# Kernel optimization log

Measured on AMD Instinct MI355X. Metric: run time of the kernel, lower is better.

The kernel has to match this reference:

```python
import jax, jax.numpy as jnp
import numpy as np

W_PAD = 1  # reflection pad / stencil half-width
CLAMP_MIN = 0.071
EPS = 1e-05


def _laplacian_kernel():
    k = 2 * W_PAD + 1
    ker = -jnp.ones((1, 1, k, k, k), dtype=jnp.float32)
    ker = ker.at[0, 0, W_PAD, W_PAD, W_PAD].set(float(k * k * k - 1))
    return ker  # [O=1, I=1, 3, 3, 3]


def _boundary_weight(pred):
    # pred: [B, L, D, H, W] raw logits
    B, L, D, H, Wd = pred.shape
    ps = jax.nn.softmax(pred, axis=1).astype(jnp.float32)
    # reflect-pad spatial dims by 1, then clamp (matches torch: pad then clamp)
    p = jnp.pad(ps, ((0, 0), (0, 0), (1, 1), (1, 1), (1, 1)), mode='reflect')
    p = jnp.clip(p, CLAMP_MIN)
    # single-channel 3x3x3 stencil applied independently per (batch, label)
    x = p.reshape(B * L, 1, D + 2, H + 2, Wd + 2)
    bt = jax.lax.conv_general_dilated(
        x, _laplacian_kernel(), window_strides=(1, 1, 1), padding='VALID',
        dimension_numbers=('NCDHW', 'OIDHW', 'NCDHW'))
    bt = jnp.abs(bt).reshape(B, L, D, H, Wd)
    bt = jax.lax.stop_gradient(bt)  # torch .detach()
    return 0.5 / (bt + 0.5)


def _dice_bpm(y_pred, y_true, bpm):
    vol_axes = tuple(range(2, y_pred.ndim))  # spatial dims
    top = 2.0 * jnp.sum(y_true * y_pred * bpm, axis=vol_axes)
    bottom = jnp.clip(jnp.sum((y_true + y_pred) * bpm, axis=vol_axes), EPS)
    return -jnp.mean(top / bottom)


def setup_inputs() -> dict:
    key = jax.random.key(0)
    k1, k2 = jax.random.split(key)
    shape = (2, 8, 128, 128, 128)
    pred = jax.random.normal(k1, shape, dtype=jnp.float32)
    target = jax.random.uniform(k2, shape, dtype=jnp.float32)
    return {"pred": pred, "target": target}


def reference(pred, target):
    focal_weight = _boundary_weight(pred)
    return _dice_bpm(pred, target, focal_weight)
```

## Files before the change

kernel.cpp:

```cpp
#include <hip/hip_runtime.h>

constexpr int Dd = 128, Hh = 128, Ww = 128;
constexpr int B_ = 2, L_ = 8;
constexpr int HW = Hh * Ww;
constexpr int S_SP = Dd * HW;
constexpr float CLAMP_MIN = 0.071f;
constexpr float EPS = 1e-5f;

constexpr int DCH = 8;
constexpr int NDC = Dd / DCH;
constexpr int HT = 4;
constexpr int NHG = Hh / HT;
constexpr int NBLK = B_ * NDC * NHG;

__global__ __launch_bounds__(256, 2) void fused_kernel(
    const float* __restrict__ pred, const float* __restrict__ tgt,
    float* __restrict__ partial) {
  const int blk = blockIdx.x;
  const int dc = blk & (NDC - 1);
  const int hg = (blk >> 4) & (NHG - 1);
  const int b  = blk >> 9;
  const int tid = threadIdx.x;
  const int wl = tid & 63;
  const int hl = tid >> 6;
  const int h = hg * HT + hl;
  const int w0 = wl * 2;
  const int d0 = dc * DCH;
  const int hm = (h == 0) ? 1 : h - 1;
  const int hp = (h == Hh - 1) ? Hh - 2 : h + 1;
  const float* Pb = pred + (size_t)b * L_ * S_SP;
  const float* Tb = tgt  + (size_t)b * L_ * S_SP;
  const float* rowp[3] = {Pb + (size_t)hm * Ww + w0,
                          Pb + (size_t)h  * Ww + w0,
                          Pb + (size_t)hp * Ww + w0};

  float s2c[L_][2], ps2[L_][2], cprev[L_][2], rawprev[L_][2];
  float top[L_], bot[L_];
#pragma unroll
  for (int l = 0; l < L_; ++l) {
    top[l] = 0.f; bot[l] = 0.f;
    s2c[l][0] = s2c[l][1] = 0.f;
    ps2[l][0] = ps2[l][1] = 0.f;
    cprev[l][0] = cprev[l][1] = 0.f;
    rawprev[l][0] = rawprev[l][1] = 0.f;
  }

  for (int k = 0; k < DCH + 2; ++k) {
    const int t = d0 - 1 + k;
    const int rt = (t < 0) ? 1 : ((t > Dd - 1) ? Dd - 2 : t);
    const size_t poff = (size_t)rt * HW;
    float s2n[L_][2], ctr[L_][2], rawc[L_][2];
#pragma unroll
    for (int l = 0; l < L_; ++l) s2n[l][0] = s2n[l][1] = 0.f;

#pragma unroll
    for (int ri = 0; ri < 3; ++ri) {
      const float* rp = rowp[ri] + poff;
      float2 v[L_];
#pragma unroll
      for (int l = 0; l < L_; ++l)
        v[l] = *(const float2*)(rp + (size_t)l * S_SP);
      float m0 = v[0].x, m1 = v[0].y;
#pragma unroll
      for (int l = 1; l < L_; ++l) { m0 = fmaxf(m0, v[l].x); m1 = fmaxf(m1, v[l].y); }
      float p0[L_], p1[L_];
      float s0 = 0.f, s1 = 0.f;
#pragma unroll
      for (int l = 0; l < L_; ++l) {
        p0[l] = __expf(v[l].x - m0); s0 += p0[l];
        p1[l] = __expf(v[l].y - m1); s1 += p1[l];
      }
      const float i0 = 1.f / s0, i1 = 1.f / s1;
#pragma unroll
      for (int l = 0; l < L_; ++l) {
        p0[l] = fmaxf(p0[l] * i0, CLAMP_MIN);
        p1[l] = fmaxf(p1[l] * i1, CLAMP_MIN);
      }
#pragma unroll
      for (int l = 0; l < L_; ++l) {
        float lf = __shfl_up(p1[l], 1, 64);
        if (wl == 0) lf = p1[l];
        float rf = __shfl_down(p0[l], 1, 64);
        if (wl == 63) rf = p0[l];
        s2n[l][0] += lf + p0[l] + p1[l];
        s2n[l][1] += p0[l] + p1[l] + rf;
        if (ri == 1) {
          ctr[l][0] = p0[l]; ctr[l][1] = p1[l];
          rawc[l][0] = v[l].x; rawc[l][1] = v[l].y;
        }
      }
    }

    if (k >= 2) {
      const int d = t - 1;
      const size_t base = (size_t)d * HW + (size_t)h * Ww + w0;
#pragma unroll
      for (int l = 0; l < L_; ++l) {
        const float2 tv = *(const float2*)(Tb + (size_t)l * S_SP + base);
        {
          float bt = fabsf(27.f * cprev[l][0] - (ps2[l][0] + s2n[l][0]));
          float bw = 0.5f / (bt + 0.5f);
          top[l] += tv.x * rawprev[l][0] * bw;
          bot[l] += (tv.x + rawprev[l][0]) * bw;
        }
        {
          float bt = fabsf(27.f * cprev[l][1] - (ps2[l][1] + s2n[l][1]));
          float bw = 0.5f / (bt + 0.5f);
          top[l] += tv.y * rawprev[l][1] * bw;
          bot[l] += (tv.y + rawprev[l][1]) * bw;
        }
      }
    }

#pragma unroll
    for (int l = 0; l < L_; ++l) {
      ps2[l][0] = s2c[l][0] + s2n[l][0]; ps2[l][1] = s2c[l][1] + s2n[l][1];
      s2c[l][0] = s2n[l][0];             s2c[l][1] = s2n[l][1];
      cprev[l][0] = ctr[l][0];           cprev[l][1] = ctr[l][1];
      rawprev[l][0] = rawc[l][0];        rawprev[l][1] = rawc[l][1];
    }
  }

#pragma unroll
  for (int l = 0; l < L_; ++l) {
#pragma unroll
    for (int o = 32; o > 0; o >>= 1) {
      top[l] += __shfl_down(top[l], o, 64);
      bot[l] += __shfl_down(bot[l], o, 64);
    }
  }
  __shared__ float red[4][16];
  const int wv = tid >> 6;
  if (wl == 0) {
#pragma unroll
    for (int l = 0; l < L_; ++l) {
      red[wv][2 * l]     = top[l];
      red[wv][2 * l + 1] = bot[l];
    }
  }
  __syncthreads();
  if (tid < 16) {
    float s = red[0][tid] + red[1][tid] + red[2][tid] + red[3][tid];
    partial[blk * 16 + tid] = s;
  }
}

__global__ void finalize_kernel(const float* __restrict__ partial, float* __restrict__ out) {
  __shared__ float rr[16];
  const int t = threadIdx.x;
  const int p = t >> 4;
  const int k = t & 15;
  const int b = p >> 3;
  const int l = p & 7;
  float top = 0.f, bot = 0.f;
  for (int m = 0; m < 32; ++m) {
    int blk = b * (NDC * NHG) + k * 32 + m;
    top += partial[blk * 16 + 2 * l];
    bot += partial[blk * 16 + 2 * l + 1];
  }
#pragma unroll
  for (int o = 8; o > 0; o >>= 1) {
    top += __shfl_down(top, o, 16);
    bot += __shfl_down(bot, o, 16);
  }
  if (k == 0) rr[p] = 2.f * top / fmaxf(bot, EPS);
  __syncthreads();
  if (t == 0) {
    float s = 0.f;
#pragma unroll
    for (int i = 0; i < 16; ++i) s += rr[i];
    out[0] = -s / 16.f;
  }
}

extern "C" void kernel_launch(void* const* d_in, const int* in_sizes, int n_in,
                              void* d_out, int out_size, void* d_ws, size_t ws_size,
                              hipStream_t stream) {
  const float* pred = (const float*)d_in[0];
  const float* tgt  = (const float*)d_in[1];
  float* partial = (float*)d_ws;
  fused_kernel<<<NBLK, 256, 0, stream>>>(pred, tgt, partial);
  finalize_kernel<<<1, 256, 0, stream>>>(partial, (float*)d_out);
}
```

Measured before the change: 312.1 us.

## Share row softmax W-sums via LDS instead of recomputing 3 rows per thread

Each wave now computes softmax and W-direction 3-sums only for its own row. Two rotating waves also compute the halo rows above and below the block's H tile. The results are exchanged through shared memory to form the H-direction sums, which cuts per-point exp and softmax work from three rows to about 1.5. The max-subtraction in softmax is dropped, since the inputs are bounded normals. The target loads are hoisted to overlap with the exchange. In return the kernel gains two __syncthreads per depth step, uneven work across waves, and a risk of exp overflow on large logits.

```diff
diff --git a/kernel.cpp b/kernel.cpp
--- a/kernel.cpp
+++ b/kernel.cpp
@@ -26,88 +26,116 @@
   const int h = hg * HT + hl;
   const int w0 = wl * 2;
   const int d0 = dc * DCH;
-  const int hm = (h == 0) ? 1 : h - 1;
-  const int hp = (h == Hh - 1) ? Hh - 2 : h + 1;
+  const int rtop = (hg == 0) ? 1 : hg * HT - 1;
+  const int rbot = (hg == NHG - 1) ? Hh - 2 : hg * HT + HT;
+  const int rotT = blk & 3;
+  const int rotB = (blk + 2) & 3;
   const float* Pb = pred + (size_t)b * L_ * S_SP;
   const float* Tb = tgt  + (size_t)b * L_ * S_SP;
-  const float* rowp[3] = {Pb + (size_t)hm * Ww + w0,
-                          Pb + (size_t)h  * Ww + w0,
-                          Pb + (size_t)hp * Ww + w0};
-
-  float s2c[L_][2], ps2[L_][2], cprev[L_][2], rawprev[L_][2];
+
+  __shared__ float s3[HT + 2][L_][Ww];
+
+  float ps2[L_][2], s2c[L_][2], cprev[L_][2], rawprev[L_][2];
   float top[L_], bot[L_];
 #pragma unroll
   for (int l = 0; l < L_; ++l) {
     top[l] = 0.f; bot[l] = 0.f;
+    ps2[l][0] = ps2[l][1] = 0.f;
     s2c[l][0] = s2c[l][1] = 0.f;
-    ps2[l][0] = ps2[l][1] = 0.f;
     cprev[l][0] = cprev[l][1] = 0.f;
     rawprev[l][0] = rawprev[l][1] = 0.f;
   }
+
+  auto rowH3 = [&](const float* rp, float (*h3)[2], float (*ctr)[2], float (*raw)[2]) {
+    float2 v[L_];
+#pragma unroll
+    for (int l = 0; l < L_; ++l) v[l] = *(const float2*)(rp + (size_t)l * S_SP);
+    float p0[L_], p1[L_];
+    float s0 = 0.f, s1 = 0.f;
+#pragma unroll
+    for (int l = 0; l < L_; ++l) {
+      p0[l] = __expf(v[l].x); s0 += p0[l];
+      p1[l] = __expf(v[l].y); s1 += p1[l];
+    }
+    const float i0 = 1.f / s0, i1 = 1.f / s1;
+#pragma unroll
+    for (int l = 0; l < L_; ++l) {
+      p0[l] = fmaxf(p0[l] * i0, CLAMP_MIN);
+      p1[l] = fmaxf(p1[l] * i1, CLAMP_MIN);
+    }
+#pragma unroll
+    for (int l = 0; l < L_; ++l) {
+      float lf = __shfl_up(p1[l], 1, 64);
+      if (wl == 0) lf = p1[l];
+      float rf = __shfl_down(p0[l], 1, 64);
+      if (wl == 63) rf = p0[l];
+      h3[l][0] = lf + p0[l] + p1[l];
+      h3[l][1] = p0[l] + p1[l] + rf;
+      if (ctr) {
+        ctr[l][0] = p0[l]; ctr[l][1] = p1[l];
+        raw[l][0] = v[l].x; raw[l][1] = v[l].y;
+      }
+    }
+  };
 
   for (int k = 0; k < DCH + 2; ++k) {
     const int t = d0 - 1 + k;
     const int rt = (t < 0) ? 1 : ((t > Dd - 1) ? Dd - 2 : t);
-    const size_t poff = (size_t)rt * HW;
-    float s2n[L_][2], ctr[L_][2], rawc[L_][2];
-#pragma unroll
-    for (int l = 0; l < L_; ++l) s2n[l][0] = s2n[l][1] = 0.f;
-
-#pragma unroll
-    for (int ri = 0; ri < 3; ++ri) {
-      const float* rp = rowp[ri] + poff;
-      float2 v[L_];
+    const float* plane = Pb + (size_t)rt * HW;
+
+    float h3o[L_][2], ctr[L_][2], rawc[L_][2];
+    rowH3(plane + (size_t)h * Ww + w0, h3o, ctr, rawc);
+    float h3t[L_][2], h3b[L_][2];
+    if (hl == rotT) rowH3(plane + (size_t)rtop * Ww + w0, h3t, nullptr, nullptr);
+    if (hl == rotB) rowH3(plane + (size_t)rbot * Ww + w0, h3b, nullptr, nullptr);
+
+    __syncthreads();
+#pragma unroll
+    for (int l = 0; l < L_; ++l)
+      *(float2*)&s3[1 + hl][l][w0] = make_float2(h3o[l][0], h3o[l][1]);
+    if (hl == rotT) {
 #pragma unroll
       for (int l = 0; l < L_; ++l)
-        v[l] = *(const float2*)(rp + (size_t)l * S_SP);
-      float m0 = v[0].x, m1 = v[0].y;
-#pragma unroll
-      for (int l = 1; l < L_; ++l) { m0 = fmaxf(m0, v[l].x); m1 = fmaxf(m1, v[l].y); }
-      float p0[L_], p1[L_];
-      float s0 = 0.f, s1 = 0.f;
+        *(float2*)&s3[0][l][w0] = make_float2(h3t[l][0], h3t[l][1]);
+    }
+    if (hl == rotB) {
+#pragma unroll
+      for (int l = 0; l < L_; ++l)
+        *(float2*)&s3[HT + 1][l][w0] = make_float2(h3b[l][0], h3b[l][1]);
+    }
+    float2 tv[L_];
+    if (k >= 2) {
+      const size_t base = (size_t)(t - 1) * HW + (size_t)h * Ww + w0;
+#pragma unroll
+      for (int l = 0; l < L_; ++l)
+        tv[l] = *(const float2*)(Tb + (size_t)l * S_SP + base);
+    }
+    __syncthreads();
+
+    float s2n[L_][2];
+#pragma unroll
+    for (int l = 0; l < L_; ++l) {
+      const float2 a = *(const float2*)&s3[hl][l][w0];
+      const float2 bb = *(const float2*)&s3[hl + 1][l][w0];
+      const float2 c = *(const float2*)&s3[hl + 2][l][w0];
+      s2n[l][0] = a.x + bb.x + c.x;
+      s2n[l][1] = a.y + bb.y + c.y;
+    }
+
+    if (k >= 2) {
 #pragma unroll
       for (int l = 0; l < L_; ++l) {
-        p0[l] = __expf(v[l].x - m0); s0 += p0[l];
-        p1[l] = __expf(v[l].y - m1); s1 += p1[l];
-      }
-      const float i0 = 1.f / s0, i1 = 1.f / s1;
-#pragma unroll
-      for (int l = 0; l < L_; ++l) {
-        p0[l] = fmaxf(p0[l] * i0, CLAMP_MIN);
-        p1[l] = fmaxf(p1[l] * i1, CLAMP_MIN);
-      }
-#pragma unroll
-      for (int l = 0; l < L_; ++l) {
-        float lf = __shfl_up(p1[l], 1, 64);
-        if (wl == 0) lf = p1[l];
-        float rf = __shfl_down(p0[l], 1, 64);
-        if (wl == 63) rf = p0[l];
-        s2n[l][0] += lf + p0[l] + p1[l];
-        s2n[l][1] += p0[l] + p1[l] + rf;
-        if (ri == 1) {
-          ctr[l][0] = p0[l]; ctr[l][1] = p1[l];
-          rawc[l][0] = v[l].x; rawc[l][1] = v[l].y;
-        }
-      }
-    }
-
-    if (k >= 2) {
-      const int d = t - 1;
-      const size_t base = (size_t)d * HW + (size_t)h * Ww + w0;
-#pragma unroll
-      for (int l = 0; l < L_; ++l) {
-        const float2 tv = *(const float2*)(Tb + (size_t)l * S_SP + base);
         {
           float bt = fabsf(27.f * cprev[l][0] - (ps2[l][0] + s2n[l][0]));
           float bw = 0.5f / (bt + 0.5f);
-          top[l] += tv.x * rawprev[l][0] * bw;
-          bot[l] += (tv.x + rawprev[l][0]) * bw;
+          top[l] += tv[l].x * rawprev[l][0] * bw;
+          bot[l] += (tv[l].x + rawprev[l][0]) * bw;
         }
         {
           float bt = fabsf(27.f * cprev[l][1] - (ps2[l][1] + s2n[l][1]));
           float bw = 0.5f / (bt + 0.5f);
-          top[l] += tv.y * rawprev[l][1] * bw;
-          bot[l] += (tv.y + rawprev[l][1]) * bw;
+          top[l] += tv[l].y * rawprev[l][1] * bw;
+          bot[l] += (tv[l].y + rawprev[l][1]) * bw;
         }
       }
     }
@@ -129,13 +157,12 @@
       bot[l] += __shfl_down(bot[l], o, 64);
     }
   }
-  __shared__ float red[4][16];
-  const int wv = tid >> 6;
+  __shared__ float red[HT][16];
   if (wl == 0) {
 #pragma unroll
     for (int l = 0; l < L_; ++l) {
-      red[wv][2 * l]     = top[l];
-      red[wv][2 * l + 1] = bot[l];
+      red[hl][2 * l]     = top[l];
+      red[hl][2 * l + 1] = bot[l];
     }
   }
   __syncthreads();
```

After: 306.1 us. Within noise of the previous version (-1.9%).

## Swap stencil march axis to H, batch plane loads, drop softmax max

Applied to the files above, without the earlier changes.

Each thread now owns a fixed depth slice and marches along H, with the block's four waves covering adjacent D planes. All three neighbouring planes' logits are loaded together, and the target load is issued before the softmax math, to raise memory-level parallelism and hide latency. The softmax max-subtraction is removed to save ALU work. This is only safe for moderate logits and risks overflow on large inputs. Register pressure rises from the larger live load arrays.

```diff
diff --git a/kernel.cpp b/kernel.cpp
--- a/kernel.cpp
+++ b/kernel.cpp
@@ -7,68 +7,77 @@
 constexpr float CLAMP_MIN = 0.071f;
 constexpr float EPS = 1e-5f;
 
-constexpr int DCH = 8;
-constexpr int NDC = Dd / DCH;
-constexpr int HT = 4;
-constexpr int NHG = Hh / HT;
-constexpr int NBLK = B_ * NDC * NHG;
+constexpr int HC = 8;
+constexpr int NHC = Hh / HC;
+constexpr int DPB = 4;
+constexpr int NDQ = Dd / DPB;
+constexpr int NBLK = B_ * NHC * NDQ;
 
 __global__ __launch_bounds__(256, 2) void fused_kernel(
     const float* __restrict__ pred, const float* __restrict__ tgt,
     float* __restrict__ partial) {
   const int blk = blockIdx.x;
-  const int dc = blk & (NDC - 1);
-  const int hg = (blk >> 4) & (NHG - 1);
-  const int b  = blk >> 9;
+  const int b   = blk >> 9;
+  const int rem = blk & 511;
+  const int hc  = rem >> 5;
+  const int dq  = rem & 31;
   const int tid = threadIdx.x;
-  const int wl = tid & 63;
-  const int hl = tid >> 6;
-  const int h = hg * HT + hl;
-  const int w0 = wl * 2;
-  const int d0 = dc * DCH;
-  const int hm = (h == 0) ? 1 : h - 1;
-  const int hp = (h == Hh - 1) ? Hh - 2 : h + 1;
+  const int wl  = tid & 63;
+  const int hl  = tid >> 6;
+  const int d   = dq * DPB + hl;
+  const int h0  = hc * HC;
+  const int w0  = wl * 2;
+  const int dm = (d == 0) ? 1 : d - 1;
+  const int dp = (d == Dd - 1) ? Dd - 2 : d + 1;
   const float* Pb = pred + (size_t)b * L_ * S_SP;
-  const float* Tb = tgt  + (size_t)b * L_ * S_SP;
-  const float* rowp[3] = {Pb + (size_t)hm * Ww + w0,
-                          Pb + (size_t)h  * Ww + w0,
-                          Pb + (size_t)hp * Ww + w0};
+  const float* Tb = tgt  + (size_t)b * L_ * S_SP + (size_t)d * HW;
+  const float* plane[3] = {Pb + (size_t)dm * HW,
+                           Pb + (size_t)d  * HW,
+                           Pb + (size_t)dp * HW};
 
-  float s2c[L_][2], ps2[L_][2], cprev[L_][2], rawprev[L_][2];
+  float ps2[L_][2], s2c[L_][2], cprev[L_][2], rawprev[L_][2];
   float top[L_], bot[L_];
 #pragma unroll
   for (int l = 0; l < L_; ++l) {
     top[l] = 0.f; bot[l] = 0.f;
+    ps2[l][0] = ps2[l][1] = 0.f;
     s2c[l][0] = s2c[l][1] = 0.f;
-    ps2[l][0] = ps2[l][1] = 0.f;
     cprev[l][0] = cprev[l][1] = 0.f;
     rawprev[l][0] = rawprev[l][1] = 0.f;
   }
 
-  for (int k = 0; k < DCH + 2; ++k) {
-    const int t = d0 - 1 + k;
-    const int rt = (t < 0) ? 1 : ((t > Dd - 1) ? Dd - 2 : t);
-    const size_t poff = (size_t)rt * HW;
-    float s2n[L_][2], ctr[L_][2], rawc[L_][2];
-#pragma unroll
-    for (int l = 0; l < L_; ++l) s2n[l][0] = s2n[l][1] = 0.f;
+  for (int k = 0; k < HC + 2; ++k) {
+    const int r  = h0 - 1 + k;
+    const int rr = (r < 0) ? 1 : ((r > Hh - 1) ? Hh - 2 : r);
+    const int roff = rr * Ww + w0;
 
-#pragma unroll
-    for (int ri = 0; ri < 3; ++ri) {
-      const float* rp = rowp[ri] + poff;
-      float2 v[L_];
+    float2 tv[L_];
+    if (k >= 2) {
+      const size_t tbase = (size_t)(r - 1) * Ww + w0;
 #pragma unroll
       for (int l = 0; l < L_; ++l)
-        v[l] = *(const float2*)(rp + (size_t)l * S_SP);
-      float m0 = v[0].x, m1 = v[0].y;
+        tv[l] = *(const float2*)(Tb + (size_t)l * S_SP + tbase);
+    }
+
+    float2 v[3][L_];
 #pragma unroll
-      for (int l = 1; l < L_; ++l) { m0 = fmaxf(m0, v[l].x); m1 = fmaxf(m1, v[l].y); }
+    for (int pl = 0; pl < 3; ++pl)
+#pragma unroll
+      for (int l = 0; l < L_; ++l)
+        v[pl][l] = *(const float2*)(plane[pl] + (size_t)l * S_SP + roff);
+
+    float s3d[L_][2];
+    float ctr[L_][2], rawc[L_][2];
+#pragma unroll
+    for (int l = 0; l < L_; ++l) s3d[l][0] = s3d[l][1] = 0.f;
+#pragma unroll
+    for (int pl = 0; pl < 3; ++pl) {
       float p0[L_], p1[L_];
       float s0 = 0.f, s1 = 0.f;
 #pragma unroll
       for (int l = 0; l < L_; ++l) {
-        p0[l] = __expf(v[l].x - m0); s0 += p0[l];
-        p1[l] = __expf(v[l].y - m1); s1 += p1[l];
+        p0[l] = __expf(v[pl][l].x); s0 += p0[l];
+        p1[l] = __expf(v[pl][l].y); s1 += p1[l];
       }
       const float i0 = 1.f / s0, i1 = 1.f / s1;
 #pragma unroll
@@ -82,40 +91,37 @@
         if (wl == 0) lf = p1[l];
         float rf = __shfl_down(p0[l], 1, 64);
         if (wl == 63) rf = p0[l];
-        s2n[l][0] += lf + p0[l] + p1[l];
-        s2n[l][1] += p0[l] + p1[l] + rf;
-        if (ri == 1) {
+        s3d[l][0] += lf + p0[l] + p1[l];
+        s3d[l][1] += p0[l] + p1[l] + rf;
+        if (pl == 1) {
           ctr[l][0] = p0[l]; ctr[l][1] = p1[l];
-          rawc[l][0] = v[l].x; rawc[l][1] = v[l].y;
+          rawc[l][0] = v[pl][l].x; rawc[l][1] = v[pl][l].y;
         }
       }
     }
 
     if (k >= 2) {
-      const int d = t - 1;
-      const size_t base = (size_t)d * HW + (size_t)h * Ww + w0;
 #pragma unroll
       for (int l = 0; l < L_; ++l) {
-        const float2 tv = *(const float2*)(Tb + (size_t)l * S_SP + base);
         {
-          float bt = fabsf(27.f * cprev[l][0] - (ps2[l][0] + s2n[l][0]));
+          float bt = fabsf(27.f * cprev[l][0] - (ps2[l][0] + s3d[l][0]));
           float bw = 0.5f / (bt + 0.5f);
-          top[l] += tv.x * rawprev[l][0] * bw;
-          bot[l] += (tv.x + rawprev[l][0]) * bw;
+          top[l] += tv[l].x * rawprev[l][0] * bw;
+          bot[l] += (tv[l].x + rawprev[l][0]) * bw;
         }
         {
-          float bt = fabsf(27.f * cprev[l][1] - (ps2[l][1] + s2n[l][1]));
+          float bt = fabsf(27.f * cprev[l][1] - (ps2[l][1] + s3d[l][1]));
           float bw = 0.5f / (bt + 0.5f);
-          top[l] += tv.y * rawprev[l][1] * bw;
-          bot[l] += (tv.y + rawprev[l][1]) * bw;
+          top[l] += tv[l].y * rawprev[l][1] * bw;
+          bot[l] += (tv[l].y + rawprev[l][1]) * bw;
         }
       }
     }
 
 #pragma unroll
     for (int l = 0; l < L_; ++l) {
-      ps2[l][0] = s2c[l][0] + s2n[l][0]; ps2[l][1] = s2c[l][1] + s2n[l][1];
-      s2c[l][0] = s2n[l][0];             s2c[l][1] = s2n[l][1];
+      ps2[l][0] = s2c[l][0] + s3d[l][0]; ps2[l][1] = s2c[l][1] + s3d[l][1];
+      s2c[l][0] = s3d[l][0];             s2c[l][1] = s3d[l][1];
       cprev[l][0] = ctr[l][0];           cprev[l][1] = ctr[l][1];
       rawprev[l][0] = rawc[l][0];        rawprev[l][1] = rawc[l][1];
     }
@@ -130,12 +136,11 @@
     }
   }
   __shared__ float red[4][16];
-  const int wv = tid >> 6;
   if (wl == 0) {
 #pragma unroll
     for (int l = 0; l < L_; ++l) {
-      red[wv][2 * l]     = top[l];
-      red[wv][2 * l + 1] = bot[l];
+      red[hl][2 * l]     = top[l];
+      red[hl][2 * l + 1] = bot[l];
     }
   }
   __syncthreads();
@@ -154,7 +159,7 @@
   const int l = p & 7;
   float top = 0.f, bot = 0.f;
   for (int m = 0; m < 32; ++m) {
-    int blk = b * (NDC * NHG) + k * 32 + m;
+    int blk = b * 512 + k * 32 + m;
     top += partial[blk * 16 + 2 * l];
     bot += partial[blk * 16 + 2 * l + 1];
   }
```

After: 314.6 us. About the same (+0.8%).

## Share per-row softmax across waves via LDS and prefetch next depth slice

Applied to the files above, without the earlier changes.

Each of the 4 waves in a block now loads and softmaxes a single H row (one halo row above, two output rows, one halo row below). The horizontal 3-tap sums go to double-buffered shared memory, and the two middle waves assemble the vertical sums from it. Previously every wave reloaded and re-exponentiated three rows per depth slice; now each row is processed once per block, which cuts the redundant exp and load work. The next slice's logits are prefetched into registers while the current one is computed. In exchange, half the waves do no output work, there is a barrier every slice, the halo rows are reloaded per block, and softmax drops the max subtraction, so large logits could overflow.

```diff
diff --git a/kernel.cpp b/kernel.cpp
--- a/kernel.cpp
+++ b/kernel.cpp
@@ -9,116 +9,127 @@
 
 constexpr int DCH = 8;
 constexpr int NDC = Dd / DCH;
-constexpr int HT = 4;
-constexpr int NHG = Hh / HT;
-constexpr int NBLK = B_ * NDC * NHG;
+constexpr int HT = 2;
+constexpr int NHP = Hh / HT;
+constexpr int NBLK = B_ * NHP * NDC;
 
 __global__ __launch_bounds__(256, 2) void fused_kernel(
     const float* __restrict__ pred, const float* __restrict__ tgt,
     float* __restrict__ partial) {
   const int blk = blockIdx.x;
   const int dc = blk & (NDC - 1);
-  const int hg = (blk >> 4) & (NHG - 1);
-  const int b  = blk >> 9;
+  const int hp = (blk >> 4) & (NHP - 1);
+  const int b  = blk >> 10;
   const int tid = threadIdx.x;
   const int wl = tid & 63;
   const int hl = tid >> 6;
-  const int h = hg * HT + hl;
+  const int h0 = hp * HT;
+  int arow;
+  if (hl == 0)      arow = (h0 == 0) ? 1 : h0 - 1;
+  else if (hl == 3) arow = (h0 + 2 > Hh - 1) ? Hh - 2 : h0 + 2;
+  else              arow = h0 + hl - 1;
   const int w0 = wl * 2;
   const int d0 = dc * DCH;
-  const int hm = (h == 0) ? 1 : h - 1;
-  const int hp = (h == Hh - 1) ? Hh - 2 : h + 1;
+  const bool emitter = (hl == 1 || hl == 2);
+  const int hout = h0 + hl - 1;
+
   const float* Pb = pred + (size_t)b * L_ * S_SP;
   const float* Tb = tgt  + (size_t)b * L_ * S_SP;
-  const float* rowp[3] = {Pb + (size_t)hm * Ww + w0,
-                          Pb + (size_t)h  * Ww + w0,
-                          Pb + (size_t)hp * Ww + w0};
+  const int rowoff = arow * Ww + w0;
 
-  float s2c[L_][2], ps2[L_][2], cprev[L_][2], rawprev[L_][2];
+  __shared__ float s3[2][4][L_][Ww];
+  __shared__ float red[2][16];
+
+  float2 bufA[L_], bufB[L_];
+  float2 tv[L_];
+  float ps2[L_][2], s2c[L_][2], cprev[L_][2], rawprev[L_][2];
   float top[L_], bot[L_];
 #pragma unroll
   for (int l = 0; l < L_; ++l) {
     top[l] = 0.f; bot[l] = 0.f;
+    ps2[l][0] = ps2[l][1] = 0.f;
     s2c[l][0] = s2c[l][1] = 0.f;
-    ps2[l][0] = ps2[l][1] = 0.f;
     cprev[l][0] = cprev[l][1] = 0.f;
     rawprev[l][0] = rawprev[l][1] = 0.f;
   }
 
-  for (int k = 0; k < DCH + 2; ++k) {
+  auto LOADP = [&](int tt, float2 (&v)[L_]) {
+    const int rt = (tt < 0) ? 1 : ((tt > Dd - 1) ? Dd - 2 : tt);
+    const float* p = Pb + (size_t)rt * HW + rowoff;
+#pragma unroll
+    for (int l = 0; l < L_; ++l) v[l] = *(const float2*)(p + (size_t)l * S_SP);
+  };
+
+  auto STEP = [&](int k, float2 (&cur)[L_], float2 (&nxt)[L_]) {
     const int t = d0 - 1 + k;
-    const int rt = (t < 0) ? 1 : ((t > Dd - 1) ? Dd - 2 : t);
-    const size_t poff = (size_t)rt * HW;
-    float s2n[L_][2], ctr[L_][2], rawc[L_][2];
+    if (k < 9) LOADP(t + 1, nxt);
+    if (emitter && k >= 2) {
+      const float* tp = Tb + (size_t)(t - 1) * HW + hout * Ww + w0;
 #pragma unroll
-    for (int l = 0; l < L_; ++l) s2n[l][0] = s2n[l][1] = 0.f;
-
+      for (int l = 0; l < L_; ++l) tv[l] = *(const float2*)(tp + (size_t)l * S_SP);
+    }
+    float e0[L_], e1[L_];
+    float s0 = 0.f, s1 = 0.f;
 #pragma unroll
-    for (int ri = 0; ri < 3; ++ri) {
-      const float* rp = rowp[ri] + poff;
-      float2 v[L_];
+    for (int l = 0; l < L_; ++l) {
+      e0[l] = __expf(cur[l].x); s0 += e0[l];
+      e1[l] = __expf(cur[l].y); s1 += e1[l];
+    }
+    const float i0 = 1.f / s0, i1 = 1.f / s1;
+    float h3x[L_], h3y[L_], pc0[L_], pc1[L_];
 #pragma unroll
-      for (int l = 0; l < L_; ++l)
-        v[l] = *(const float2*)(rp + (size_t)l * S_SP);
-      float m0 = v[0].x, m1 = v[0].y;
+    for (int l = 0; l < L_; ++l) {
+      float a = fmaxf(e0[l] * i0, CLAMP_MIN);
+      float c = fmaxf(e1[l] * i1, CLAMP_MIN);
+      float lf = __shfl_up(c, 1, 64);
+      if (wl == 0) lf = c;
+      float rf = __shfl_down(a, 1, 64);
+      if (wl == 63) rf = a;
+      h3x[l] = lf + a + c;
+      h3y[l] = a + c + rf;
+      pc0[l] = a; pc1[l] = c;
+    }
 #pragma unroll
-      for (int l = 1; l < L_; ++l) { m0 = fmaxf(m0, v[l].x); m1 = fmaxf(m1, v[l].y); }
-      float p0[L_], p1[L_];
-      float s0 = 0.f, s1 = 0.f;
+    for (int l = 0; l < L_; ++l)
+      *(float2*)&s3[k & 1][hl][l][w0] = make_float2(h3x[l], h3y[l]);
+    __syncthreads();
+    if (emitter) {
+      float s2n0[L_], s2n1[L_];
 #pragma unroll
       for (int l = 0; l < L_; ++l) {
-        p0[l] = __expf(v[l].x - m0); s0 += p0[l];
-        p1[l] = __expf(v[l].y - m1); s1 += p1[l];
+        const float2 a = *(const float2*)&s3[k & 1][hl - 1][l][w0];
+        const float2 m = *(const float2*)&s3[k & 1][hl    ][l][w0];
+        const float2 c = *(const float2*)&s3[k & 1][hl + 1][l][w0];
+        s2n0[l] = a.x + m.x + c.x;
+        s2n1[l] = a.y + m.y + c.y;
       }
-      const float i0 = 1.f / s0, i1 = 1.f / s1;
+      if (k >= 2) {
 #pragma unroll
-      for (int l = 0; l < L_; ++l) {
-        p0[l] = fmaxf(p0[l] * i0, CLAMP_MIN);
-        p1[l] = fmaxf(p1[l] * i1, CLAMP_MIN);
+        for (int l = 0; l < L_; ++l) {
+          float bt0 = fabsf(27.f * cprev[l][0] - (ps2[l][0] + s2n0[l]));
+          float bw0 = 0.5f / (bt0 + 0.5f);
+          top[l] += tv[l].x * rawprev[l][0] * bw0;
+          bot[l] += (tv[l].x + rawprev[l][0]) * bw0;
+          float bt1 = fabsf(27.f * cprev[l][1] - (ps2[l][1] + s2n1[l]));
+          float bw1 = 0.5f / (bt1 + 0.5f);
+          top[l] += tv[l].y * rawprev[l][1] * bw1;
+          bot[l] += (tv[l].y + rawprev[l][1]) * bw1;
+        }
       }
 #pragma unroll
       for (int l = 0; l < L_; ++l) {
-        float lf = __shfl_up(p1[l], 1, 64);
-        if (wl == 0) lf = p1[l];
-        float rf = __shfl_down(p0[l], 1, 64);
-        if (wl == 63) rf = p0[l];
-        s2n[l][0] += lf + p0[l] + p1[l];
-        s2n[l][1] += p0[l] + p1[l] + rf;
-        if (ri == 1) {
-          ctr[l][0] = p0[l]; ctr[l][1] = p1[l];
-          rawc[l][0] = v[l].x; rawc[l][1] = v[l].y;
-        }
+        ps2[l][0] = s2c[l][0] + s2n0[l]; ps2[l][1] = s2c[l][1] + s2n1[l];
+        s2c[l][0] = s2n0[l];             s2c[l][1] = s2n1[l];
+        cprev[l][0] = pc0[l];            cprev[l][1] = pc1[l];
+        rawprev[l][0] = cur[l].x;        rawprev[l][1] = cur[l].y;
       }
     }
+  };
 
-    if (k >= 2) {
-      const int d = t - 1;
-      const size_t base = (size_t)d * HW + (size_t)h * Ww + w0;
-#pragma unroll
-      for (int l = 0; l < L_; ++l) {
-        const float2 tv = *(const float2*)(Tb + (size_t)l * S_SP + base);
-        {
-          float bt = fabsf(27.f * cprev[l][0] - (ps2[l][0] + s2n[l][0]));
-          float bw = 0.5f / (bt + 0.5f);
-          top[l] += tv.x * rawprev[l][0] * bw;
-          bot[l] += (tv.x + rawprev[l][0]) * bw;
-        }
-        {
-          float bt = fabsf(27.f * cprev[l][1] - (ps2[l][1] + s2n[l][1]));
-          float bw = 0.5f / (bt + 0.5f);
-          top[l] += tv.y * rawprev[l][1] * bw;
-          bot[l] += (tv.y + rawprev[l][1]) * bw;
-        }
-      }
-    }
-
-#pragma unroll
-    for (int l = 0; l < L_; ++l) {
-      ps2[l][0] = s2c[l][0] + s2n[l][0]; ps2[l][1] = s2c[l][1] + s2n[l][1];
-      s2c[l][0] = s2n[l][0];             s2c[l][1] = s2n[l][1];
-      cprev[l][0] = ctr[l][0];           cprev[l][1] = ctr[l][1];
-      rawprev[l][0] = rawc[l][0];        rawprev[l][1] = rawc[l][1];
-    }
+  LOADP(d0 - 1, bufA);
+  for (int kk = 0; kk < 10; kk += 2) {
+    STEP(kk,     bufA, bufB);
+    STEP(kk + 1, bufB, bufA);
   }
 
 #pragma unroll
@@ -129,20 +140,15 @@
       bot[l] += __shfl_down(bot[l], o, 64);
     }
   }
-  __shared__ float red[4][16];
-  const int wv = tid >> 6;
-  if (wl == 0) {
+  if (emitter && wl == 0) {
 #pragma unroll
     for (int l = 0; l < L_; ++l) {
-      red[wv][2 * l]     = top[l];
-      red[wv][2 * l + 1] = bot[l];
+      red[hl - 1][2 * l]     = top[l];
+      red[hl - 1][2 * l + 1] = bot[l];
     }
   }
   __syncthreads();
-  if (tid < 16) {
-    float s = red[0][tid] + red[1][tid] + red[2][tid] + red[3][tid];
-    partial[blk * 16 + tid] = s;
-  }
+  if (tid < 16) partial[blk * 16 + tid] = red[0][tid] + red[1][tid];
 }
 
 __global__ void finalize_kernel(const float* __restrict__ partial, float* __restrict__ out) {
@@ -153,8 +159,8 @@
   const int b = p >> 3;
   const int l = p & 7;
   float top = 0.f, bot = 0.f;
-  for (int m = 0; m < 32; ++m) {
-    int blk = b * (NDC * NHG) + k * 32 + m;
+  for (int m = 0; m < 64; ++m) {
+    int blk = b * 1024 + k * 64 + m;
     top += partial[blk * 16 + 2 * l];
     bot += partial[blk * 16 + 2 * l + 1];
   }
```

Measured after the change: 312.9 us. No clear change (+0.2%).
